# Kernel optimization log

Hardware: AMD Instinct MI355X
Metric: run time of the kernel (lower is better)

The kernel has to match this reference:

```python
import jax, jax.numpy as jnp
import numpy as np

B, A, C = 8, 19206, 91          # batch, anchors, classes (incl. background at idx 0)
K = 256                          # pre-NMS top-k candidates per class
MAX_DET = 100                    # max detections per class and final per image
IOU_T = 0.6                      # NMS IoU threshold
SCALES = (10.0, 10.0, 5.0, 5.0)


def decode_boxes(enc, anchors):
    # enc: [B,A,4] (ty,tx,th,tw); anchors: [A,4] (yc,xc,h,w) -> corners [B,A,4]
    ty = enc[..., 0] / SCALES[0]
    tx = enc[..., 1] / SCALES[1]
    th = enc[..., 2] / SCALES[2]
    tw = enc[..., 3] / SCALES[3]
    ya, xa, ha, wa = anchors[:, 0], anchors[:, 1], anchors[:, 2], anchors[:, 3]
    yc = ty * ha + ya
    xc = tx * wa + xa
    h = jnp.exp(th) * ha
    w = jnp.exp(tw) * wa
    return jnp.stack([yc - h / 2, xc - w / 2, yc + h / 2, xc + w / 2], axis=-1)


def iou_matrix(b):
    # b: [K,4] corners -> [K,K] IoU
    area = (b[:, 2] - b[:, 0]) * (b[:, 3] - b[:, 1])
    tl = jnp.maximum(b[:, None, :2], b[None, :, :2])
    br = jnp.minimum(b[:, None, 2:], b[None, :, 2:])
    wh = jnp.clip(br - tl, 0.0)
    inter = wh[..., 0] * wh[..., 1]
    union = area[:, None] + area[None, :] - inter
    return inter / jnp.maximum(union, 1e-8)


def nms_single(boxes, scores):
    # boxes [K,4], scores [K] (sigmoid scores, >0). Greedy NMS, MAX_DET picks.
    iou = iou_matrix(boxes)

    def step(s, _):
        i = jnp.argmax(s)
        val = s[i]
        keep = val > 0.0  # suppressed entries are set to -1
        s_new = jnp.where(iou[i] >= IOU_T, -1.0, s)
        return s_new, (i, jnp.where(keep, val, 0.0), keep)

    _, (idx, vals, valid) = jax.lax.scan(step, scores, None, length=MAX_DET)
    sel_boxes = boxes[idx] * valid[:, None].astype(boxes.dtype)
    return sel_boxes, vals, valid


def reference(box_encodings, class_logits, anchors):
    decoded = decode_boxes(box_encodings, anchors)            # [B,A,4]
    scores = jax.nn.sigmoid(class_logits)[..., 1:]            # drop background: [B,A,C-1]
    sc = jnp.transpose(scores, (0, 2, 1))                     # [B,C-1,A]
    top_s, top_i = jax.lax.top_k(sc, K)                       # [B,C-1,K]
    boxes_sel = jnp.take_along_axis(decoded[:, None], top_i[..., None], axis=2)  # [B,C-1,K,4]
    sel_boxes, sel_scores, _ = jax.vmap(jax.vmap(nms_single))(boxes_sel, top_s)  # [B,C-1,MAX_DET,*]
    Cc = C - 1
    cls = jnp.broadcast_to(
        jnp.arange(1, C, dtype=decoded.dtype)[None, :, None], (B, Cc, MAX_DET))
    flat_scores = sel_scores.reshape(B, -1)                   # [B,(C-1)*MAX_DET]
    flat_boxes = sel_boxes.reshape(B, -1, 4)
    flat_cls = cls.reshape(B, -1)
    fin_s, fin_i = jax.lax.top_k(flat_scores, MAX_DET)        # [B,MAX_DET]
    fin_boxes = jnp.take_along_axis(flat_boxes, fin_i[..., None], axis=1)
    fin_cls = jnp.take_along_axis(flat_cls, fin_i, axis=1)
    # detections: [boxes(4), class(1), score(1)] -> [B,MAX_DET,6]
    return jnp.concatenate([fin_boxes, fin_cls[..., None], fin_s[..., None]], axis=2)


def setup_inputs() -> dict:
    key = jax.random.key(0)
    k1, k2, k3 = jax.random.split(key, 3)
    box_encodings = jax.random.normal(k1, (B, A, 4), dtype=jnp.float32)
    class_logits = jax.random.normal(k2, (B, A, C), dtype=jnp.float32)
    anchors = jax.random.uniform(k3, (A, 4), dtype=jnp.float32)  # yc,xc,h,w in (0,1)
    return {"box_encodings": box_encodings, "class_logits": class_logits, "anchors": anchors}
```

## Files before the change

kernel.cpp:

```cpp
#include <hip/hip_runtime.h>
#include <stdint.h>
#include <math.h>

typedef unsigned int u32;
typedef unsigned long long u64;
typedef unsigned char u8;

#define BB 8
#define AA 19206
#define CCH 91
#define NCLS 90
#define KSEL 256
#define MAXDET 100
#define NROWS (BB*NCLS)
#define NFLAT (NCLS*MAXDET)
#define IOU_T 0.6f

#define ATILE 64
__global__ void __launch_bounds__(256) k_sigT(const float* __restrict__ logits,
    float* __restrict__ sc, u8* __restrict__ sbin, int b0) {
  __shared__ __align__(16) float tile[ATILE * CCH];
  int bl = blockIdx.y;
  int b  = b0 + bl;
  int a0 = blockIdx.x * ATILE;
  int nt = AA - a0; if (nt > ATILE) nt = ATILE;
  int nload = nt * CCH;
  const float* src = logits + ((size_t)b * AA + a0) * CCH;
  const float2* s2 = (const float2*)src;
  int n2 = nload >> 1;
  for (int i = threadIdx.x; i < n2; i += 256) ((float2*)tile)[i] = s2[i];
  __syncthreads();
  for (int j = threadIdx.x; j < ATILE * NCLS; j += 256) {
    int c  = j >> 6;
    int ai = j & 63;
    if (ai < nt) {
      float x = tile[ai * CCH + (c + 1)];
      float s = 1.0f / (1.0f + expf(-x));
      size_t o = ((size_t)bl * NCLS + c) * AA + a0 + ai;
      sc[o] = s;
      sbin[o] = (u8)min(255, (int)(s * 256.0f));
    }
  }
}

__global__ void __launch_bounds__(512) k_row(const float* __restrict__ sc,
    const u8* __restrict__ sbin,
    float* __restrict__ tks, int* __restrict__ tki, int row0) {
  __shared__ u32 hist[256];
  __shared__ u32 suf[256];
  __shared__ u64 cand[512];
  __shared__ int shBs, ctr;
  int rl  = blockIdx.x;
  int row = row0 + rl;
  int tid = threadIdx.x;
  const float2* src = (const float2*)(sc + (size_t)rl * AA);
  const uchar2* sb2 = (const uchar2*)(sbin + (size_t)rl * AA);
  if (tid < 256) hist[tid] = 0;
  if (tid == 0) ctr = 0;
  __syncthreads();
  for (int i = tid; i < AA / 2; i += 512) {
    uchar2 bb = sb2[i];
    atomicAdd(&hist[bb.x], 1u);
    atomicAdd(&hist[bb.y], 1u);
  }
  __syncthreads();
  if (tid < 256) suf[tid] = hist[tid];
  __syncthreads();
  for (int off = 1; off < 256; off <<= 1) {
    u32 v = 0;
    if (tid < 256 && tid + off < 256) v = suf[tid + off];
    __syncthreads();
    if (tid < 256) suf[tid] += v;
    __syncthreads();
  }
  if (tid < 256) {
    u32 nxt = (tid < 255) ? suf[tid + 1] : 0u;
    if (suf[tid] >= (u32)KSEL && nxt < (u32)KSEL) shBs = tid;
  }
  __syncthreads();
  int Bs = shBs;
  int lane = tid & 63;
  for (int i = tid; i < AA / 2; i += 512) {
    float2 v = src[i];
    {
      bool p = min(255, (int)(v.x * 256.0f)) >= Bs;
      u64 m = __ballot(p);
      if (p) {
        int leader = (int)(__ffsll((long long)m) - 1);
        int base = 0;
        if (lane == leader) base = atomicAdd(&ctr, (int)__popcll(m));
        base = __shfl(base, leader);
        int pos = base + (int)__popcll(m & ((1ull << lane) - 1ull));
        if (pos < 512)
          cand[pos] = ((u64)__float_as_uint(v.x) << 32) | (u32)(~(u32)(2 * i));
      }
    }
    {
      bool p = min(255, (int)(v.y * 256.0f)) >= Bs;
      u64 m = __ballot(p);
      if (p) {
        int leader = (int)(__ffsll((long long)m) - 1);
        int base = 0;
        if (lane == leader) base = atomicAdd(&ctr, (int)__popcll(m));
        base = __shfl(base, leader);
        int pos = base + (int)__popcll(m & ((1ull << lane) - 1ull));
        if (pos < 512)
          cand[pos] = ((u64)__float_as_uint(v.y) << 32) | (u32)(~(u32)(2 * i + 1));
      }
    }
  }
  __syncthreads();
  int n = ctr < 512 ? ctr : 512;
  for (int i = n + tid; i < 512; i += 512) cand[i] = 0;
  __syncthreads();
  for (int k = 2; k <= 512; k <<= 1) {
    for (int j = k >> 1; j > 0; j >>= 1) {
      int l = tid ^ j;
      if (l > tid) {
        u64 x = cand[tid], y = cand[l];
        bool asc = ((tid & k) == 0);
        if ((x > y) == asc) { cand[tid] = y; cand[l] = x; }
      }
      __syncthreads();
    }
  }
  if (tid < KSEL) {
    u64 kk = cand[511 - tid];
    tks[(size_t)row * KSEL + tid] = __uint_as_float((u32)(kk >> 32));
    tki[(size_t)row * KSEL + tid] = (int)(~(u32)kk);
  }
}

__device__ inline float rdlane(float x, int l) {
  return __int_as_float(__builtin_amdgcn_readlane(__float_as_int(x), l));
}

__device__ inline float4 decode1(const float* __restrict__ enc,
                                 const float* __restrict__ anch, int b, int ai) {
  float4 e  = ((const float4*)enc)[(size_t)b * AA + ai];
  float4 an = ((const float4*)anch)[ai];
  float ty = e.x / 10.0f, tx = e.y / 10.0f, th = e.z / 5.0f, tw = e.w / 5.0f;
  float yc = ty * an.z + an.x;
  float xc = tx * an.w + an.y;
  float h  = expf(th) * an.z;
  float w  = expf(tw) * an.w;
  float4 o;
  o.x = yc - h * 0.5f; o.y = xc - w * 0.5f; o.z = yc + h * 0.5f; o.w = xc + w * 0.5f;
  return o;
}

__global__ void __launch_bounds__(256) k_nms(const float* __restrict__ enc,
    const float* __restrict__ anch,
    const float* __restrict__ tks, const int* __restrict__ tki,
    float* __restrict__ flat_s, float* __restrict__ flat_b) {
  int wid = threadIdx.x >> 6, lane = threadIdx.x & 63;
  int row = blockIdx.x * 4 + wid;
  int b = row / NCLS, c = row % NCLS;
  const float* trow = tks + (size_t)row * KSEL;
  const int*   irow = tki + (size_t)row * KSEL;
  float s0 = trow[lane], s1 = trow[64 + lane], s2 = trow[128 + lane], s3 = trow[192 + lane];
  int   i0 = irow[lane], i1 = irow[64 + lane], i2 = irow[128 + lane], i3 = irow[192 + lane];
  float4 B0 = decode1(enc, anch, b, i0);
  float4 B1 = decode1(enc, anch, b, i1);
  float4 B2 = decode1(enc, anch, b, i2);
  float4 B3 = decode1(enc, anch, b, i3);
  float a0 = (B0.z - B0.x) * (B0.w - B0.y);
  float a1 = (B1.z - B1.x) * (B1.w - B1.y);
  float a2 = (B2.z - B2.x) * (B2.w - B2.y);
  float a3 = (B3.z - B3.x) * (B3.w - B3.y);
  u64 m0 = __ballot(s0 > 0.0f);
  u64 m1 = __ballot(s1 > 0.0f);
  u64 m2 = __ballot(s2 > 0.0f);
  u64 m3 = __ballot(s3 > 0.0f);
  const float cP = __uint_as_float(0x3F199999u);
  const double M = 0.5 * ((double)cP + (double)0.6f);
  float ss0 = 0.0f, ss1 = 0.0f;
  float4 ob0; ob0.x = ob0.y = ob0.z = ob0.w = 0.0f;
  float4 ob1 = ob0;
  size_t fo = (size_t)b * NFLAT + (size_t)c * MAXDET;
  for (int d = 0; d < MAXDET; d++) {
    int kw; u64 w;
    if      (m0) { kw = 0; w = m0; }
    else if (m1) { kw = 1; w = m1; }
    else if (m2) { kw = 2; w = m2; }
    else if (m3) { kw = 3; w = m3; }
    else break;
    int lw = (int)__builtin_ctzll(w);
    float sw_, wx_, wy_, wz_, ww_;
    if (kw == 0) {
      sw_ = rdlane(s0, lw);
      wx_ = rdlane(B0.x, lw); wy_ = rdlane(B0.y, lw);
      wz_ = rdlane(B0.z, lw); ww_ = rdlane(B0.w, lw);
    } else if (kw == 1) {
      sw_ = rdlane(s1, lw);
      wx_ = rdlane(B1.x, lw); wy_ = rdlane(B1.y, lw);
      wz_ = rdlane(B1.z, lw); ww_ = rdlane(B1.w, lw);
    } else if (kw == 2) {
      sw_ = rdlane(s2, lw);
      wx_ = rdlane(B2.x, lw); wy_ = rdlane(B2.y, lw);
      wz_ = rdlane(B2.z, lw); ww_ = rdlane(B2.w, lw);
    } else {
      sw_ = rdlane(s3, lw);
      wx_ = rdlane(B3.x, lw); wy_ = rdlane(B3.y, lw);
      wz_ = rdlane(B3.z, lw); ww_ = rdlane(B3.w, lw);
    }
    bool c0 = (lane == d);
    bool c1 = (lane + 64 == d);
    ss0 = c0 ? sw_ : ss0;
    ob0.x = c0 ? wx_ : ob0.x; ob0.y = c0 ? wy_ : ob0.y;
    ob0.z = c0 ? wz_ : ob0.z; ob0.w = c0 ? ww_ : ob0.w;
    ss1 = c1 ? sw_ : ss1;
    ob1.x = c1 ? wx_ : ob1.x; ob1.y = c1 ? wy_ : ob1.y;
    ob1.z = c1 ? wz_ : ob1.z; ob1.w = c1 ? ww_ : ob1.w;
    float ia = (wz_ - wx_) * (ww_ - wy_);
    float in0, in1, in2, in3, un0, un1, un2, un3;
#define PAIR(BX, AK, INK, UNK) { \
      float ty = fmaxf(wx_, BX.x), tx = fmaxf(wy_, BX.y); \
      float by = fminf(wz_, BX.z), bw = fminf(ww_, BX.w); \
      float hh = fmaxf(by - ty, 0.0f), wvv = fmaxf(bw - tx, 0.0f); \
      INK = hh * wvv; \
      UNK = fmaxf(ia + AK - INK, 1e-8f); }
    PAIR(B0, a0, in0, un0)
    PAIR(B1, a1, in1, un1)
    PAIR(B2, a2, in2, un2)
    PAIR(B3, a3, in3, un3)
#undef PAIR
    u64 cm0 = __ballot((double)in0 >= M * (double)un0);
    u64 cm1 = __ballot((double)in1 >= M * (double)un1);
    u64 cm2 = __ballot((double)in2 >= M * (double)un2);
    u64 cm3 = __ballot((double)in3 >= M * (double)un3);
    m0 &= ~cm0; m1 &= ~cm1; m2 &= ~cm2; m3 &= ~cm3;
  }
  flat_s[fo + lane] = ss0;
  ((float4*)flat_b)[fo + lane] = ob0;
  if (lane < MAXDET - 64) {
    flat_s[fo + 64 + lane] = ss1;
    ((float4*)flat_b)[fo + 64 + lane] = ob1;
  }
}

__device__ inline void bitonic_u64_asc(u64* a, int n, int tid) {
  for (int k = 2; k <= n; k <<= 1) {
    for (int j = k >> 1; j > 0; j >>= 1) {
      for (int i = tid; i < n; i += 256) {
        int l = i ^ j;
        if (l > i) {
          u64 x = a[i], y = a[l];
          bool asc = ((i & k) == 0);
          if ((x > y) == asc) { a[i] = y; a[l] = x; }
        }
      }
      __syncthreads();
    }
  }
}
__device__ inline void bitonic_u32_asc(u32* a, int n, int tid) {
  for (int k = 2; k <= n; k <<= 1) {
    for (int j = k >> 1; j > 0; j >>= 1) {
      for (int i = tid; i < n; i += 256) {
        int l = i ^ j;
        if (l > i) {
          u32 x = a[i], y = a[l];
          bool asc = ((i & k) == 0);
          if ((x > y) == asc) { a[i] = y; a[l] = x; }
        }
      }
      __syncthreads();
    }
  }
}

template<typename F>
__device__ inline void radix_select(F getv, int n, int kwant,
    u32* hist, u32* suf, int* sh2, int tid,
    u32& V_out, int& GT_out, int& r_out) {
  int r = kwant; u32 V = 0; int GT = 0;
  for (int lvl = 0; lvl < 3; lvl++) {
    int shift = (lvl == 0) ? 19 : ((lvl == 1) ? 8 : 0);
    int nbins = (lvl == 2) ? 256 : 2048;
    for (int i = tid; i < nbins; i += 256) hist[i] = 0;
    __syncthreads();
    for (int idx = tid; idx < n; idx += 256) {
      u32 u = __float_as_uint(getv(idx));
      bool ok = (lvl == 0) || (lvl == 1 ? ((u >> 19) == (V >> 19))
                                        : ((u >> 8)  == (V >> 8)));
      u64 zm = __ballot(ok && u == 0u);
      if (ok) {
        if (u == 0u) {
          if ((int)(threadIdx.x & 63) == (int)(__ffsll((long long)zm) - 1))
            atomicAdd(&hist[0], (u32)__popcll(zm));
        } else {
          atomicAdd(&hist[(u >> shift) & (u32)(nbins - 1)], 1u);
        }
      }
    }
    __syncthreads();
    int G = nbins >> 8;
    u32 ps = 0;
    for (int g = 0; g < G; g++) ps += hist[tid * G + g];
    suf[tid] = ps;
    __syncthreads();
    for (int off = 1; off < 256; off <<= 1) {
      u32 v = (tid + off < 256) ? suf[tid + off] : 0u;
      __syncthreads();
      suf[tid] += v;
      __syncthreads();
    }
    u32 sufnext = (tid < 255) ? suf[tid + 1] : 0u;
    if (suf[tid] >= (u32)r && sufnext < (u32)r) {
      u32 cum = sufnext; int kb = tid * G;
      for (int bin = tid * G + G - 1; bin >= tid * G; bin--) {
        cum += hist[bin];
        if (cum >= (u32)r) { kb = bin; break; }
      }
      sh2[0] = kb;
      sh2[1] = (int)(cum - hist[kb]);
    }
    __syncthreads();
    int kb = sh2[0], gt = sh2[1];
    r -= gt; GT += gt; V |= ((u32)kb) << shift;
    __syncthreads();
  }
  V_out = V; GT_out = GT; r_out = r;
}

__global__ void __launch_bounds__(256) k_topk_direct(const float* __restrict__ src,
    float* __restrict__ tks, int* __restrict__ tki) {
  __shared__ u32 hist[2048];
  __shared__ u32 suf[256];
  __shared__ int sh2[2];
  __shared__ u64 sel[KSEL];
  __shared__ u32 tie[512];
  __shared__ int cgt, ctie;
  int row = blockIdx.x, tid = threadIdx.x;
  int b = row / NCLS, c = row % NCLS;
  const float* base = src + (size_t)b * AA * CCH + (c + 1);
  auto getv = [&](int i) -> float {
    float x = base[(size_t)i * CCH]; return 1.0f / (1.0f + expf(-x));
  };
  u32 V; int GT, r;
  radix_select(getv, AA, KSEL, hist, suf, sh2, tid, V, GT, r);
  if (tid == 0) { cgt = 0; ctie = 0; }
  __syncthreads();
  for (int i = tid; i < AA; i += 256) {
    u32 u = __float_as_uint(getv(i));
    if (u > V) {
      int p = atomicAdd(&cgt, 1);
      sel[p] = ((u64)u << 32) | (u32)(~(u32)i);
    } else if (u == V) {
      int p = atomicAdd(&ctie, 1);
      if (p < 512) tie[p] = (u32)i;
    }
  }
  __syncthreads();
  int nt = ctie < 512 ? ctie : 512;
  for (int i = tid + nt; i < 512; i += 256) tie[i] = 0xFFFFFFFFu;
  __syncthreads();
  bitonic_u32_asc(tie, 512, tid);
  for (int i = tid; i < r; i += 256)
    sel[GT + i] = ((u64)V << 32) | (u32)(~tie[i]);
  __syncthreads();
  bitonic_u64_asc(sel, KSEL, tid);
  for (int j = tid; j < KSEL; j += 256) {
    u64 kk = sel[KSEL - 1 - j];
    tks[(size_t)row * KSEL + j] = __uint_as_float((u32)(kk >> 32));
    tki[(size_t)row * KSEL + j] = (int)(~(u32)kk);
  }
}

__global__ void __launch_bounds__(512) k_final(const float* __restrict__ flat_s,
    const float* __restrict__ flat_b, float* __restrict__ out) {
  __shared__ u32 hist[256];
  __shared__ u32 suf[256];
  __shared__ u64 cand[512];
  __shared__ int shBs, ctr;
  int b = blockIdx.x, tid = threadIdx.x;
  int lane = tid & 63;
  const float2* src = (const float2*)(flat_s + (size_t)b * NFLAT);
  if (tid < 256) hist[tid] = 0;
  if (tid == 0) ctr = 0;
  __syncthreads();
  for (int i = tid; i < NFLAT / 2; i += 512) {
    float2 v = src[i];
    atomicAdd(&hist[min(255, (int)(v.x * 256.0f))], 1u);
    atomicAdd(&hist[min(255, (int)(v.y * 256.0f))], 1u);
  }
  __syncthreads();
  if (tid < 256) suf[tid] = hist[tid];
  __syncthreads();
  for (int off = 1; off < 256; off <<= 1) {
    u32 v = 0;
    if (tid < 256 && tid + off < 256) v = suf[tid + off];
    __syncthreads();
    if (tid < 256) suf[tid] += v;
    __syncthreads();
  }
  if (tid < 256) {
    u32 nxt = (tid < 255) ? suf[tid + 1] : 0u;
    if (suf[tid] >= (u32)MAXDET && nxt < (u32)MAXDET) shBs = tid;
  }
  __syncthreads();
  int Bs = shBs;
  for (int i = tid; i < NFLAT / 2; i += 512) {
    float2 v = src[i];
    {
      bool p = min(255, (int)(v.x * 256.0f)) >= Bs;
      u64 m = __ballot(p);
      if (p) {
        int leader = (int)(__ffsll((long long)m) - 1);
        int base = 0;
        if (lane == leader) base = atomicAdd(&ctr, (int)__popcll(m));
        base = __shfl(base, leader);
        int pos = base + (int)__popcll(m & ((1ull << lane) - 1ull));
        if (pos < 512)
          cand[pos] = ((u64)__float_as_uint(v.x) << 32) | (u32)(~(u32)(2 * i));
      }
    }
    {
      bool p = min(255, (int)(v.y * 256.0f)) >= Bs;
      u64 m = __ballot(p);
      if (p) {
        int leader = (int)(__ffsll((long long)m) - 1);
        int base = 0;
        if (lane == leader) base = atomicAdd(&ctr, (int)__popcll(m));
        base = __shfl(base, leader);
        int pos = base + (int)__popcll(m & ((1ull << lane) - 1ull));
        if (pos < 512)
          cand[pos] = ((u64)__float_as_uint(v.y) << 32) | (u32)(~(u32)(2 * i + 1));
      }
    }
  }
  __syncthreads();
  int n = ctr < 512 ? ctr : 512;
  for (int i = n + tid; i < 512; i += 512) cand[i] = 0;
  __syncthreads();
  for (int k = 2; k <= 512; k <<= 1) {
    for (int j = k >> 1; j > 0; j >>= 1) {
      int l = tid ^ j;
      if (l > tid) {
        u64 x = cand[tid], y = cand[l];
        bool asc = ((tid & k) == 0);
        if ((x > y) == asc) { cand[tid] = y; cand[l] = x; }
      }
      __syncthreads();
    }
  }
  if (tid < MAXDET) {
    u64 kk = cand[511 - tid];
    u32 u  = (u32)(kk >> 32);
    int fi = (int)(~(u32)kk);
    float4 bb = ((const float4*)flat_b)[(size_t)b * NFLAT + fi];
    float* o = out + ((size_t)b * MAXDET + tid) * 6;
    o[0] = bb.x; o[1] = bb.y; o[2] = bb.z; o[3] = bb.w;
    o[4] = (float)(fi / 100 + 1);
    o[5] = __uint_as_float(u);
  }
}

extern "C" void kernel_launch(void* const* d_in, const int* in_sizes, int n_in,
                              void* d_out, int out_size, void* d_ws, size_t ws_size,
                              hipStream_t stream) {
  const float* enc    = (const float*)d_in[0];
  const float* logits = (const float*)d_in[1];
  const float* anch   = (const float*)d_in[2];
  float* out = (float*)d_out;
  char* ws = (char*)d_ws;

  size_t off = 0;
  auto alloc = [&](size_t bytes) {
    size_t o = off;
    off += (bytes + 255) & ~(size_t)255;
    return o;
  };
  size_t o_tks  = alloc((size_t)NROWS * KSEL * 4);
  size_t o_tki  = alloc((size_t)NROWS * KSEL * 4);
  size_t o_fls  = alloc((size_t)BB * NFLAT * 4);
  size_t o_flb  = alloc((size_t)BB * NFLAT * 16);
  size_t need_base = off;
  size_t o_sc = off;
  size_t per_batch_sc   = ((size_t)NCLS * AA * 4 + 255) & ~(size_t)255;
  size_t per_batch_sbin = ((size_t)NCLS * AA + 255) & ~(size_t)255;

  int CB = 0;
  for (int cb = BB; cb >= 1; cb >>= 1) {
    if (ws_size >= need_base + (size_t)cb * (per_batch_sc + per_batch_sbin)) {
      CB = cb; break;
    }
  }

  float* tks = (float*)(ws + o_tks);
  int*   tki = (int*)  (ws + o_tki);
  float* fls = (float*)(ws + o_fls);
  float* flb = (float*)(ws + o_flb);
  float* scp = (float*)(ws + o_sc);
  u8*    sbp = (u8*)   (ws + o_sc + (size_t)CB * per_batch_sc);

  if (CB > 0) {
    for (int b0 = 0; b0 < BB; b0 += CB) {
      hipLaunchKernelGGL(k_sigT, dim3((AA + ATILE - 1) / ATILE, CB), dim3(256), 0,
                         stream, logits, scp, sbp, b0);
      hipLaunchKernelGGL(k_row, dim3(NCLS * CB), dim3(512), 0, stream,
                         scp, sbp, tks, tki, b0 * NCLS);
    }
  } else {
    hipLaunchKernelGGL(k_topk_direct, dim3(NROWS), dim3(256), 0, stream,
                       logits, tks, tki);
  }
  hipLaunchKernelGGL(k_nms, dim3(NROWS / 4), dim3(256), 0, stream,
                     enc, anch, tks, tki, fls, flb);
  hipLaunchKernelGGL(k_final, dim3(BB), dim3(512), 0, stream,
                     fls, flb, out);
}
```

Before: 113.3 us.

## Speculatively pick two NMS winners per iteration in wave-level greedy loop

The greedy NMS loop now selects the top surviving candidate and also the next one, computing IoU of both against all candidates in the same iteration. If the second candidate is not suppressed by the first, both are committed and the loop advances by two, roughly halving the serial iteration count. In exchange each iteration does twice the IoU and ballot work and adds selects with more register pressure, and the gain depends on how often the second pick survives.

```diff
diff --git a/kernel.cpp b/kernel.cpp
--- a/kernel.cpp
+++ b/kernel.cpp
@@ -178,58 +178,95 @@
   float4 ob0; ob0.x = ob0.y = ob0.z = ob0.w = 0.0f;
   float4 ob1 = ob0;
   size_t fo = (size_t)b * NFLAT + (size_t)c * MAXDET;
-  for (int d = 0; d < MAXDET; d++) {
-    int kw; u64 w;
-    if      (m0) { kw = 0; w = m0; }
-    else if (m1) { kw = 1; w = m1; }
-    else if (m2) { kw = 2; w = m2; }
-    else if (m3) { kw = 3; w = m3; }
+  int d = 0;
+  while (d < MAXDET) {
+    int kw1; u64 w;
+    if      (m0) { kw1 = 0; w = m0; }
+    else if (m1) { kw1 = 1; w = m1; }
+    else if (m2) { kw1 = 2; w = m2; }
+    else if (m3) { kw1 = 3; w = m3; }
     else break;
-    int lw = (int)__builtin_ctzll(w);
-    float sw_, wx_, wy_, wz_, ww_;
-    if (kw == 0) {
-      sw_ = rdlane(s0, lw);
-      wx_ = rdlane(B0.x, lw); wy_ = rdlane(B0.y, lw);
-      wz_ = rdlane(B0.z, lw); ww_ = rdlane(B0.w, lw);
-    } else if (kw == 1) {
-      sw_ = rdlane(s1, lw);
-      wx_ = rdlane(B1.x, lw); wy_ = rdlane(B1.y, lw);
-      wz_ = rdlane(B1.z, lw); ww_ = rdlane(B1.w, lw);
-    } else if (kw == 2) {
-      sw_ = rdlane(s2, lw);
-      wx_ = rdlane(B2.x, lw); wy_ = rdlane(B2.y, lw);
-      wz_ = rdlane(B2.z, lw); ww_ = rdlane(B2.w, lw);
-    } else {
-      sw_ = rdlane(s3, lw);
-      wx_ = rdlane(B3.x, lw); wy_ = rdlane(B3.y, lw);
-      wz_ = rdlane(B3.z, lw); ww_ = rdlane(B3.w, lw);
-    }
-    bool c0 = (lane == d);
-    bool c1 = (lane + 64 == d);
-    ss0 = c0 ? sw_ : ss0;
-    ob0.x = c0 ? wx_ : ob0.x; ob0.y = c0 ? wy_ : ob0.y;
-    ob0.z = c0 ? wz_ : ob0.z; ob0.w = c0 ? ww_ : ob0.w;
-    ss1 = c1 ? sw_ : ss1;
-    ob1.x = c1 ? wx_ : ob1.x; ob1.y = c1 ? wy_ : ob1.y;
-    ob1.z = c1 ? wz_ : ob1.z; ob1.w = c1 ? ww_ : ob1.w;
-    float ia = (wz_ - wx_) * (ww_ - wy_);
-    float in0, in1, in2, in3, un0, un1, un2, un3;
-#define PAIR(BX, AK, INK, UNK) { \
-      float ty = fmaxf(wx_, BX.x), tx = fmaxf(wy_, BX.y); \
-      float by = fminf(wz_, BX.z), bw = fminf(ww_, BX.w); \
+    int lw1 = (int)__builtin_ctzll(w);
+    u64 bit1 = 1ull << lw1;
+    u64 q0 = (kw1 == 0) ? (m0 & ~bit1) : m0;
+    u64 q1 = (kw1 == 1) ? (m1 & ~bit1) : m1;
+    u64 q2 = (kw1 == 2) ? (m2 & ~bit1) : m2;
+    u64 q3 = (kw1 == 3) ? (m3 & ~bit1) : m3;
+    bool has2 = (q0 | q1 | q2 | q3) != 0ull;
+    int kw2; u64 w2w;
+    if      (q0) { kw2 = 0; w2w = q0; }
+    else if (q1) { kw2 = 1; w2w = q1; }
+    else if (q2) { kw2 = 2; w2w = q2; }
+    else         { kw2 = 3; w2w = q3 ? q3 : 1ull; }
+    int lw2 = (int)__builtin_ctzll(w2w);
+    float cs1 = (kw1 == 0) ? s0   : (kw1 == 1) ? s1   : (kw1 == 2) ? s2   : s3;
+    float cx1 = (kw1 == 0) ? B0.x : (kw1 == 1) ? B1.x : (kw1 == 2) ? B2.x : B3.x;
+    float cy1 = (kw1 == 0) ? B0.y : (kw1 == 1) ? B1.y : (kw1 == 2) ? B2.y : B3.y;
+    float cz1 = (kw1 == 0) ? B0.z : (kw1 == 1) ? B1.z : (kw1 == 2) ? B2.z : B3.z;
+    float cw1 = (kw1 == 0) ? B0.w : (kw1 == 1) ? B1.w : (kw1 == 2) ? B2.w : B3.w;
+    float sA = rdlane(cs1, lw1);
+    float xA = rdlane(cx1, lw1);
+    float yA = rdlane(cy1, lw1);
+    float zA = rdlane(cz1, lw1);
+    float wA = rdlane(cw1, lw1);
+    float cs2 = (kw2 == 0) ? s0   : (kw2 == 1) ? s1   : (kw2 == 2) ? s2   : s3;
+    float cx2 = (kw2 == 0) ? B0.x : (kw2 == 1) ? B1.x : (kw2 == 2) ? B2.x : B3.x;
+    float cy2 = (kw2 == 0) ? B0.y : (kw2 == 1) ? B1.y : (kw2 == 2) ? B2.y : B3.y;
+    float cz2 = (kw2 == 0) ? B0.z : (kw2 == 1) ? B1.z : (kw2 == 2) ? B2.z : B3.z;
+    float cw2 = (kw2 == 0) ? B0.w : (kw2 == 1) ? B1.w : (kw2 == 2) ? B2.w : B3.w;
+    float sB = rdlane(cs2, lw2);
+    float xB = rdlane(cx2, lw2);
+    float yB = rdlane(cy2, lw2);
+    float zB = rdlane(cz2, lw2);
+    float wB = rdlane(cw2, lw2);
+    float iaA = (zA - xA) * (wA - yA);
+    float iaB = (zB - xB) * (wB - yB);
+#define PAIR(WX, WY, WZ, WW, IA, BX, AK, INK, UNK) { \
+      float ty = fmaxf(WX, BX.x), tx = fmaxf(WY, BX.y); \
+      float by = fminf(WZ, BX.z), bw = fminf(WW, BX.w); \
       float hh = fmaxf(by - ty, 0.0f), wvv = fmaxf(bw - tx, 0.0f); \
       INK = hh * wvv; \
-      UNK = fmaxf(ia + AK - INK, 1e-8f); }
-    PAIR(B0, a0, in0, un0)
-    PAIR(B1, a1, in1, un1)
-    PAIR(B2, a2, in2, un2)
-    PAIR(B3, a3, in3, un3)
+      UNK = fmaxf(IA + AK - INK, 1e-8f); }
+    float iA0, iA1, iA2, iA3, uA0, uA1, uA2, uA3;
+    float iB0, iB1, iB2, iB3, uB0, uB1, uB2, uB3;
+    PAIR(xA, yA, zA, wA, iaA, B0, a0, iA0, uA0)
+    PAIR(xA, yA, zA, wA, iaA, B1, a1, iA1, uA1)
+    PAIR(xA, yA, zA, wA, iaA, B2, a2, iA2, uA2)
+    PAIR(xA, yA, zA, wA, iaA, B3, a3, iA3, uA3)
+    PAIR(xB, yB, zB, wB, iaB, B0, a0, iB0, uB0)
+    PAIR(xB, yB, zB, wB, iaB, B1, a1, iB1, uB1)
+    PAIR(xB, yB, zB, wB, iaB, B2, a2, iB2, uB2)
+    PAIR(xB, yB, zB, wB, iaB, B3, a3, iB3, uB3)
 #undef PAIR
-    u64 cm0 = __ballot((double)in0 >= M * (double)un0);
-    u64 cm1 = __ballot((double)in1 >= M * (double)un1);
-    u64 cm2 = __ballot((double)in2 >= M * (double)un2);
-    u64 cm3 = __ballot((double)in3 >= M * (double)un3);
-    m0 &= ~cm0; m1 &= ~cm1; m2 &= ~cm2; m3 &= ~cm3;
+    u64 cA0 = __ballot((double)iA0 >= M * (double)uA0);
+    u64 cA1 = __ballot((double)iA1 >= M * (double)uA1);
+    u64 cA2 = __ballot((double)iA2 >= M * (double)uA2);
+    u64 cA3 = __ballot((double)iA3 >= M * (double)uA3);
+    u64 cB0 = __ballot((double)iB0 >= M * (double)uB0);
+    u64 cB1 = __ballot((double)iB1 >= M * (double)uB1);
+    u64 cB2 = __ballot((double)iB2 >= M * (double)uB2);
+    u64 cB3 = __ballot((double)iB3 >= M * (double)uB3);
+    u64 cA_k2 = (kw2 == 0) ? cA0 : (kw2 == 1) ? cA1 : (kw2 == 2) ? cA2 : cA3;
+    bool commit2 = has2 && (d + 1 < MAXDET) && (((cA_k2 >> lw2) & 1ull) == 0ull);
+    bool c0a = (lane == d);
+    bool c1a = (lane + 64 == d);
+    ss0 = c0a ? sA : ss0;
+    ob0.x = c0a ? xA : ob0.x; ob0.y = c0a ? yA : ob0.y;
+    ob0.z = c0a ? zA : ob0.z; ob0.w = c0a ? wA : ob0.w;
+    ss1 = c1a ? sA : ss1;
+    ob1.x = c1a ? xA : ob1.x; ob1.y = c1a ? yA : ob1.y;
+    ob1.z = c1a ? zA : ob1.z; ob1.w = c1a ? wA : ob1.w;
+    bool c0b = commit2 && (lane == d + 1);
+    bool c1b = commit2 && (lane + 64 == d + 1);
+    ss0 = c0b ? sB : ss0;
+    ob0.x = c0b ? xB : ob0.x; ob0.y = c0b ? yB : ob0.y;
+    ob0.z = c0b ? zB : ob0.z; ob0.w = c0b ? wB : ob0.w;
+    ss1 = c1b ? sB : ss1;
+    ob1.x = c1b ? xB : ob1.x; ob1.y = c1b ? yB : ob1.y;
+    ob1.z = c1b ? zB : ob1.z; ob1.w = c1b ? wB : ob1.w;
+    m0 &= ~cA0; m1 &= ~cA1; m2 &= ~cA2; m3 &= ~cA3;
+    if (commit2) { m0 &= ~cB0; m1 &= ~cB1; m2 &= ~cB2; m3 &= ~cB3; }
+    d += 1 + (commit2 ? 1 : 0);
   }
   flat_s[fo + lane] = ss0;
   ((float4*)flat_b)[fo + lane] = ob0;
```

Measured after the change: 116.5 us. 2.8% more time.
